# Optimization experiments

Measured on AMD Instinct MI355X. Metric: run time of the kernel, lower is better.

The kernel has to match this reference:

```python
import jax, jax.numpy as jnp
import numpy as np

RADIUS = 0.05
HMIN = -0.02
HMAX = 0.04
NSAMPLE = 64


def setup_inputs() -> dict:
    key = jax.random.key(0)
    k1, k2, k3, k4 = jax.random.split(key, 4)
    B, N, P, C = 2, 16384, 1024, 256
    xyz = jax.random.uniform(k1, (B, N, 3), dtype=jnp.float32)
    new_xyz = jax.random.uniform(k2, (B, P, 3), dtype=jnp.float32)
    rot = jax.random.normal(k3, (B, P, 3, 3), dtype=jnp.float32)
    features = jax.random.normal(k4, (B, C, N), dtype=jnp.float32)
    return {"xyz": xyz, "new_xyz": new_xyz, "rot": rot, "features": features}


def cylinder_query(xyz, new_xyz, rot):
    """Returns (B, P, NSAMPLE) int32 indices into the N axis of xyz.

    Faithful to the torch version: the torch code sorts all N candidates by
    distance (knn with K=N) and then top-k's a cylinder score over them; since
    the candidate set is all N points, this equals a direct top-k of the score
    over N (candidate ordering only affects float ties).
    """
    # delta = candidate point - center, in world frame: (B, P, N, 3)
    delta = xyz[:, None, :, :] - new_xyz[:, :, None, :]
    # rotate into cylinder frame: matmul(delta, rot^T) -> sum_d delta_d * rot[j, d]
    dcyl = jnp.einsum('bpnd,bpjd->bpnj', delta, rot)
    x, y, z = dcyl[..., 0], dcyl[..., 1], dcyl[..., 2]
    radial = jnp.sqrt(jnp.maximum(y * y + z * z, 0.0))
    in_cyl = (radial <= RADIUS) & (x >= HMIN) & (x <= HMAX)
    score = jnp.where(in_cyl, radial + 1e-3 * jnp.abs(x), jnp.inf)
    # smallest-score top-k via top_k on negated score
    neg_vals, pos = jax.lax.top_k(-score, NSAMPLE)  # (B, P, NSAMPLE)
    vals = -neg_vals
    # fallback: nearest point (torch uses idx_cand[..., 0], the KNN-nearest)
    d2 = jnp.sum(delta * delta, axis=-1)  # (B, P, N)
    fallback = jnp.argmin(d2, axis=-1)  # (B, P)
    no_valid = jnp.isinf(vals[..., 0])  # no point inside cylinder
    idx = jnp.where(no_valid[..., None], fallback[..., None], pos)
    return idx


def reference(xyz, new_xyz, rot, features):
    B = xyz.shape[0]
    idx = cylinder_query(xyz, new_xyz, rot)  # (B, P, S)
    # group xyz: (B, P, S, 3)
    grouped_xyz = jax.vmap(lambda p, i: p[i])(xyz, idx)
    grouped_xyz = grouped_xyz - new_xyz[:, :, None, :]
    # rotate_xyz: grouped @ rot  -> sum_d g_d * rot[d, e]
    grouped_xyz = jnp.einsum('bpsd,bpde->bpse', grouped_xyz, rot)
    grouped_xyz = jnp.transpose(grouped_xyz, (0, 3, 1, 2))  # (B, 3, P, S)
    # group features: (B, C, P, S)
    grouped_feat = jax.vmap(lambda f, i: f[:, i])(features, idx)
    return jnp.concatenate([grouped_xyz, grouped_feat], axis=1)  # (B, 3+C, P, S)
```

## Files before the change

kernel.cpp:

```cpp
#include <hip/hip_runtime.h>
#include <stdint.h>

#define B_ 2
#define N_ 16384
#define P_ 1024
#define C_ 256
#define S_ 64
#define CH_ (C_ + 3)
#define CAP_ 512

#define INF_BITS 0x7F800000u

typedef unsigned long long u64;

struct QS {
    u64 keys[CAP_];
    uint32_t hist[4][256];
    u64 red[4];
    uint32_t wsum[4];
    int vflag[128];
    int cnt;
    int sel;
    uint32_t k;
};

struct GT {
    uint32_t tileu[32][130];
};

union USmem {
    QS qs;
    GT g;
};

__device__ __forceinline__ u64 umin64(u64 a, u64 b) { return a < b ? a : b; }

__device__ __forceinline__ uint32_t f2bf(float f) {
    uint32_t x = __float_as_uint(f);
    return (x + 0x7fffu + ((x >> 16) & 1u)) >> 16;
}
__device__ __forceinline__ float bf2f(uint32_t u) { return __uint_as_float(u << 16); }

__device__ u64 block_min_u64(u64 v, u64* s_red) {
    int tid = threadIdx.x;
#pragma unroll
    for (int o = 32; o > 0; o >>= 1)
        v = umin64(v, (u64)__shfl_xor(v, o, 64));
    __syncthreads();
    if ((tid & 63) == 0) s_red[tid >> 6] = v;
    __syncthreads();
    u64 r = s_red[0];
#pragma unroll
    for (int w = 1; w < 4; ++w) r = umin64(r, s_red[w]);
    return r;
}

__device__ __forceinline__ uint32_t eval_sb(float px, float py, float pz,
                                            float cx, float cy, float cz,
                                            float r0, float r1, float r2,
                                            float r3, float r4, float r5,
                                            float r6, float r7, float r8) {
    float dx = px - cx, dy = py - cy, dz = pz - cz;
    float xr = __fadd_rn(__fadd_rn(__fmul_rn(dx, r0), __fmul_rn(dy, r1)), __fmul_rn(dz, r2));
    float yr = __fadd_rn(__fadd_rn(__fmul_rn(dx, r3), __fmul_rn(dy, r4)), __fmul_rn(dz, r5));
    float zr = __fadd_rn(__fadd_rn(__fmul_rn(dx, r6), __fmul_rn(dy, r7)), __fmul_rn(dz, r8));
    float rad2 = __fadd_rn(__fmul_rn(yr, yr), __fmul_rn(zr, zr));
    float radial = __fsqrt_rn(fmaxf(rad2, 0.0f));
    bool valid = (radial <= 0.05f) && (xr >= -0.02f) && (xr <= 0.04f);
    float score = __fadd_rn(radial, __fmul_rn(1e-3f, fabsf(xr)));
    return valid ? __float_as_uint(score) : INF_BITS;
}

__device__ __forceinline__ uint32_t score_bits(const float* __restrict__ xb, int n,
                                               float cx, float cy, float cz,
                                               float r0, float r1, float r2,
                                               float r3, float r4, float r5,
                                               float r6, float r7, float r8) {
    return eval_sb(xb[n * 3 + 0], xb[n * 3 + 1], xb[n * 3 + 2],
                   cx, cy, cz, r0, r1, r2, r3, r4, r5, r6, r7, r8);
}

__device__ void select_idx(QS& qs, const float* __restrict__ xb,
                           float cx, float cy, float cz,
                           float r0, float r1, float r2, float r3, float r4,
                           float r5, float r6, float r7, float r8,
                           int* s_out) {
    const int tid = threadIdx.x;
    const int wid = tid >> 6;
    const int v = qs.cnt;

    if (v == 0) {
        u64 fb = ~0ull;
        for (int n = tid; n < N_; n += 256) {
            float px = xb[n * 3 + 0], py = xb[n * 3 + 1], pz = xb[n * 3 + 2];
            float dx = px - cx, dy = py - cy, dz = pz - cz;
            float d2 = __fadd_rn(__fadd_rn(__fmul_rn(dx, dx), __fmul_rn(dy, dy)),
                                 __fmul_rn(dz, dz));
            fb = umin64(fb, ((u64)__float_as_uint(d2) << 32) | (unsigned)n);
        }
        u64 m = block_min_u64(fb, qs.red);
        if (tid < S_) s_out[tid] = (int)(unsigned)(m & 0xFFFFFFFFu);
    } else if (v <= 64) {
        if (tid >= v && tid < 64)
            qs.keys[tid] = 0xFFFFFFFF00000000ull | (unsigned)(0x10000 + tid);
        __syncthreads();
        u64 key = 0;
        int rank = 0;
        if (tid < 64) {
            key = qs.keys[tid];
            for (int o = 0; o < 64; ++o) rank += (qs.keys[o] < key) ? 1 : 0;
        }
        __syncthreads();
        if (tid < 64) qs.keys[rank] = key;
        __syncthreads();
        const int needed = 64 - v;
        if (tid < 64 && needed > 0) {
            bool inv0 = (qs.vflag[tid] == 0);
            u64 m0 = __ballot(inv0);
            int before0 = __popcll(m0 & ((1ull << tid) - 1ull));
            if (inv0 && before0 < needed) qs.keys[v + before0] = (unsigned)tid;
            int c0 = __popcll(m0);
            if (c0 < needed) {
                bool inv1 = (qs.vflag[64 + tid] == 0);
                u64 m1 = __ballot(inv1);
                int b1 = c0 + __popcll(m1 & ((1ull << tid) - 1ull));
                if (inv1 && b1 < needed) qs.keys[v + b1] = (unsigned)(64 + tid);
            }
        }
        __syncthreads();
        if (tid < S_) s_out[tid] = (int)(unsigned)(qs.keys[tid] & 0xFFFFFFFFu);
    } else if (v <= CAP_) {
        for (int i = tid; i < v; i += 256) {
            u64 key = qs.keys[i];
            int rank = 0;
            for (int j = 0; j < v; ++j) rank += (qs.keys[j] < key) ? 1 : 0;
            if (rank < 64) s_out[rank] = (int)(unsigned)(key & 0xFFFFFFFFu);
        }
    } else {
        uint32_t prefix = 0, mask = 0, kk = 64;
        for (int pass = 0; pass < 4; ++pass) {
            const int shift = 24 - 8 * pass;
            __syncthreads();
            qs.hist[0][tid] = 0;
            qs.hist[1][tid] = 0;
            qs.hist[2][tid] = 0;
            qs.hist[3][tid] = 0;
            __syncthreads();
            for (int n = tid; n < N_; n += 256) {
                uint32_t sb = score_bits(xb, n, cx, cy, cz, r0, r1, r2, r3, r4, r5, r6, r7, r8);
                if (sb != INF_BITS && (sb & mask) == prefix)
                    atomicAdd(&qs.hist[wid][(sb >> shift) & 255u], 1u);
            }
            __syncthreads();
            uint32_t cnt = qs.hist[0][tid] + qs.hist[1][tid] + qs.hist[2][tid] + qs.hist[3][tid];
            uint32_t x = cnt;
#pragma unroll
            for (int o = 1; o < 64; o <<= 1) {
                uint32_t y = __shfl_up(x, o, 64);
                if ((tid & 63) >= o) x += y;
            }
            if ((tid & 63) == 63) qs.wsum[wid] = x;
            __syncthreads();
            uint32_t woff = 0;
            for (int w = 0; w < wid; ++w) woff += qs.wsum[w];
            uint32_t incl = x + woff;
            uint32_t excl = incl - cnt;
            if (kk > excl && kk <= incl) {
                qs.sel = tid;
                qs.k = kk - excl;
            }
            __syncthreads();
            prefix |= ((uint32_t)qs.sel) << shift;
            mask |= 255u << shift;
            kk = qs.k;
        }
        const uint32_t T = prefix;

        __syncthreads();
        if (tid == 0) qs.cnt = 0;
        __syncthreads();
        for (int n = tid; n < N_; n += 256) {
            uint32_t sb = score_bits(xb, n, cx, cy, cz, r0, r1, r2, r3, r4, r5, r6, r7, r8);
            if (sb != INF_BITS && sb <= T) {
                int pos = atomicAdd(&qs.cnt, 1);
                if (pos < CAP_) qs.keys[pos] = ((u64)sb << 32) | (unsigned)n;
            }
        }
        __syncthreads();
        int c = qs.cnt;
        if (c > CAP_) c = CAP_;
        for (int i = tid; i < c; i += 256) {
            u64 key = qs.keys[i];
            int rank = 0;
            for (int j = 0; j < c; ++j) rank += (qs.keys[j] < key) ? 1 : 0;
            if (rank < 64) s_out[rank] = (int)(unsigned)(key & 0xFFFFFFFFu);
        }
    }
}

__global__ __launch_bounds__(256) void transpose_kernel(const float* __restrict__ feat,
                                                        ushort* __restrict__ featT) {
    int t = blockIdx.x;
    int b = t >> 10;
    int rem = t & 1023;
    int cblk = rem >> 8;
    int nblk = rem & 255;
    __shared__ float tile[64][65];
    int tid = threadIdx.x;
    for (int i = tid; i < 1024; i += 256) {
        int cy = i >> 4, nx4 = (i & 15) * 4;
        float4 v = *(const float4*)&feat[((size_t)(b * C_ + cblk * 64 + cy)) * N_ +
                                         nblk * 64 + nx4];
        tile[cy][nx4 + 0] = v.x;
        tile[cy][nx4 + 1] = v.y;
        tile[cy][nx4 + 2] = v.z;
        tile[cy][nx4 + 3] = v.w;
    }
    __syncthreads();
    for (int i = tid; i < 1024; i += 256) {
        int ny = i >> 4, c4 = i & 15;
        uint32_t lo = f2bf(tile[c4 * 4 + 0][ny]) | (f2bf(tile[c4 * 4 + 1][ny]) << 16);
        uint32_t hi = f2bf(tile[c4 * 4 + 2][ny]) | (f2bf(tile[c4 * 4 + 3][ny]) << 16);
        uint2 v;
        v.x = lo;
        v.y = hi;
        *(uint2*)&featT[((size_t)(b * N_ + nblk * 64 + ny)) * C_ + cblk * 64 + c4 * 4] = v;
    }
}

__global__ __launch_bounds__(256) void qg_kernel(const ushort* __restrict__ featT,
                                                 const float* __restrict__ features,
                                                 const float* __restrict__ xyz,
                                                 const float* __restrict__ new_xyz,
                                                 const float* __restrict__ rot,
                                                 float* __restrict__ out, int useT) {
    __shared__ USmem sm;
    __shared__ int s_idx[S_];
    const int tid = threadIdx.x;
    const int lane = tid & 63;
    const int bp = blockIdx.x;
    const int b = bp >> 10;
    const int p = bp & 1023;

    if (tid == 0) sm.qs.cnt = 0;

    const float cx = new_xyz[bp * 3 + 0];
    const float cy = new_xyz[bp * 3 + 1];
    const float cz = new_xyz[bp * 3 + 2];
    const float* R = rot + (size_t)bp * 9;
    const float r0 = R[0], r1 = R[1], r2 = R[2];
    const float r3 = R[3], r4 = R[4], r5 = R[5];
    const float r6 = R[6], r7 = R[7], r8 = R[8];

    __syncthreads();

    const float* xb = xyz + (size_t)b * N_ * 3;
    const float4* xb4 = (const float4*)xb;

    for (int it = 0; it < N_ / 1024; ++it) {
        int t4 = it * 256 + tid;
        float4 A = xb4[t4 * 3 + 0];
        float4 Bv = xb4[t4 * 3 + 1];
        float4 Cv = xb4[t4 * 3 + 2];
        int n0 = t4 * 4;

        uint32_t s0 = eval_sb(A.x, A.y, A.z, cx, cy, cz, r0, r1, r2, r3, r4, r5, r6, r7, r8);
        uint32_t s1 = eval_sb(A.w, Bv.x, Bv.y, cx, cy, cz, r0, r1, r2, r3, r4, r5, r6, r7, r8);
        uint32_t s2 = eval_sb(Bv.z, Bv.w, Cv.x, cx, cy, cz, r0, r1, r2, r3, r4, r5, r6, r7, r8);
        uint32_t s3 = eval_sb(Cv.y, Cv.z, Cv.w, cx, cy, cz, r0, r1, r2, r3, r4, r5, r6, r7, r8);

        if (it == 0 && tid < 32) {
            sm.qs.vflag[n0 + 0] = (s0 != INF_BITS) ? 1 : 0;
            sm.qs.vflag[n0 + 1] = (s1 != INF_BITS) ? 1 : 0;
            sm.qs.vflag[n0 + 2] = (s2 != INF_BITS) ? 1 : 0;
            sm.qs.vflag[n0 + 3] = (s3 != INF_BITS) ? 1 : 0;
        }
        uint32_t mn = min(min(s0, s1), min(s2, s3));
        if (__any(mn != INF_BITS)) {
            uint32_t sb[4] = {s0, s1, s2, s3};
#pragma unroll
            for (int j = 0; j < 4; ++j) {
                u64 m = __ballot(sb[j] != INF_BITS);
                if (m) {
                    int leader = __builtin_ctzll(m);
                    int cnt = __popcll(m);
                    int base = 0;
                    if (lane == leader) base = atomicAdd(&sm.qs.cnt, cnt);
                    base = __shfl(base, leader, 64);
                    if (sb[j] != INF_BITS) {
                        int pos = base + __popcll(m & ((1ull << lane) - 1ull));
                        if (pos < CAP_) sm.qs.keys[pos] = ((u64)sb[j] << 32) | (unsigned)(n0 + j);
                    }
                }
            }
        }
    }
    __syncthreads();

    select_idx(sm.qs, xb, cx, cy, cz, r0, r1, r2, r3, r4, r5, r6, r7, r8, s_idx);
    __syncthreads();

    if (tid < S_) {
        int n = s_idx[tid];
        const float* pt = xyz + ((size_t)b * N_ + n) * 3;
        float dx = pt[0] - cx;
        float dy = pt[1] - cy;
        float dz = pt[2] - cz;
        float g0 = __fadd_rn(__fadd_rn(__fmul_rn(dx, r0), __fmul_rn(dy, r3)), __fmul_rn(dz, r6));
        float g1 = __fadd_rn(__fadd_rn(__fmul_rn(dx, r1), __fmul_rn(dy, r4)), __fmul_rn(dz, r7));
        float g2 = __fadd_rn(__fadd_rn(__fmul_rn(dx, r2), __fmul_rn(dy, r5)), __fmul_rn(dz, r8));
        out[(((size_t)b * CH_ + 0) * P_ + p) * S_ + tid] = g0;
        out[(((size_t)b * CH_ + 1) * P_ + p) * S_ + tid] = g1;
        out[(((size_t)b * CH_ + 2) * P_ + p) * S_ + tid] = g2;
    }

    for (int h = 0; h < 2; ++h) {
        if (h) __syncthreads();
        if (useT) {
            for (int i = tid; i < 32 * 32; i += 256) {
                int sl = i >> 5, cq = i & 31;
                int n = s_idx[h * 32 + sl];
                uint4 v = *(const uint4*)&featT[((size_t)b * N_ + n) * C_ + cq * 8];
                *(uint4*)&sm.g.tileu[sl][cq * 4] = v;
            }
        } else {
            for (int i = tid; i < 32 * 128; i += 256) {
                int sl = i >> 7, cp = i & 127;
                int n = s_idx[h * 32 + sl];
                uint32_t u0 = f2bf(features[((size_t)b * C_ + 2 * cp + 0) * N_ + n]);
                uint32_t u1 = f2bf(features[((size_t)b * C_ + 2 * cp + 1) * N_ + n]);
                sm.g.tileu[sl][cp] = u0 | (u1 << 16);
            }
        }
        __syncthreads();
        for (int i = tid; i < (C_ / 2) * 8; i += 256) {
            int cp = i >> 3, q = i & 7;
            uint32_t u0 = sm.g.tileu[4 * q + 0][cp];
            uint32_t u1 = sm.g.tileu[4 * q + 1][cp];
            uint32_t u2 = sm.g.tileu[4 * q + 2][cp];
            uint32_t u3 = sm.g.tileu[4 * q + 3][cp];
            float4 lo, hi;
            lo.x = bf2f(u0 & 0xffffu); lo.y = bf2f(u1 & 0xffffu);
            lo.z = bf2f(u2 & 0xffffu); lo.w = bf2f(u3 & 0xffffu);
            hi.x = bf2f(u0 >> 16); hi.y = bf2f(u1 >> 16);
            hi.z = bf2f(u2 >> 16); hi.w = bf2f(u3 >> 16);
            size_t base0 = (((size_t)b * CH_ + 3 + 2 * cp) * P_ + p) * S_ + h * 32 + 4 * q;
            *(float4*)&out[base0] = lo;
            *(float4*)&out[base0 + (size_t)P_ * S_] = hi;
        }
    }
}

extern "C" void kernel_launch(void* const* d_in, const int* in_sizes, int n_in,
                              void* d_out, int out_size, void* d_ws, size_t ws_size,
                              hipStream_t stream) {
    const float* xyz = (const float*)d_in[0];
    const float* new_xyz = (const float*)d_in[1];
    const float* rot = (const float*)d_in[2];
    const float* features = (const float*)d_in[3];
    float* out = (float*)d_out;

    const size_t featT_bytes = (size_t)B_ * N_ * C_ * sizeof(ushort);
    const int useT = (ws_size >= featT_bytes) ? 1 : 0;

    ushort* featT = (ushort*)d_ws;

    if (useT) {
        transpose_kernel<<<2048, 256, 0, stream>>>(features, featT);
    }
    qg_kernel<<<B_ * P_, 256, 0, stream>>>(featT, features, xyz, new_xyz, rot, out, useT);
}
```

Measured before the change: 64.23 us.

## Add uniform grid binning to prune cylinder query candidates

Adds a bin_kernel that counting-sorts each batch's points into a 16^3 grid and records cell start offsets. The query kernel maps each cylinder's extent through the inverse rotation to a world-space box of cells and scores only the points in those cells, instead of scanning all N points per query. It falls back to the full scan when the matrix is near-singular or the box covers too many cells. It also sets launch bounds to 8 blocks per SM. The cost is an extra single-block-per-batch launch (only 2 blocks) running before the others, plus binary-search overhead and dependence on the workspace being large enough.

```diff
diff --git a/kernel.cpp b/kernel.cpp
--- a/kernel.cpp
+++ b/kernel.cpp
@@ -8,6 +8,8 @@
 #define S_ 64
 #define CH_ (C_ + 3)
 #define CAP_ 512
+#define G_ 16
+#define NC_ (G_ * G_ * G_)
 
 #define INF_BITS 0x7F800000u
 
@@ -195,6 +197,68 @@
             for (int j = 0; j < c; ++j) rank += (qs.keys[j] < key) ? 1 : 0;
             if (rank < 64) s_out[rank] = (int)(unsigned)(key & 0xFFFFFFFFu);
         }
+    }
+}
+
+__global__ __launch_bounds__(256) void bin_kernel(const float* __restrict__ xyz,
+                                                  float4* __restrict__ sortedPts,
+                                                  int* __restrict__ cellStart) {
+    __shared__ uint32_t hist[NC_];
+    __shared__ uint32_t wsum[4];
+    const int b = blockIdx.x;
+    const int tid = threadIdx.x;
+    const int lane = tid & 63, wid = tid >> 6;
+    const float* xb = xyz + (size_t)b * N_ * 3;
+
+    for (int i = tid; i < NC_; i += 256) hist[i] = 0;
+    __syncthreads();
+    for (int n = tid; n < N_; n += 256) {
+        float x = xb[n * 3 + 0], y = xb[n * 3 + 1], z = xb[n * 3 + 2];
+        int cx = min(max((int)(x * 16.0f), 0), 15);
+        int cy = min(max((int)(y * 16.0f), 0), 15);
+        int cz = min(max((int)(z * 16.0f), 0), 15);
+        atomicAdd(&hist[(cx * 16 + cy) * 16 + cz], 1u);
+    }
+    __syncthreads();
+    uint32_t vals[16];
+    uint32_t s = 0;
+#pragma unroll
+    for (int k = 0; k < 16; ++k) vals[k] = hist[tid * 16 + k];
+#pragma unroll
+    for (int k = 0; k < 16; ++k) {
+        uint32_t t = vals[k];
+        vals[k] = s;
+        s += t;
+    }
+    uint32_t x = s;
+#pragma unroll
+    for (int o = 1; o < 64; o <<= 1) {
+        uint32_t y = __shfl_up(x, o, 64);
+        if (lane >= o) x += y;
+    }
+    if (lane == 63) wsum[wid] = x;
+    __syncthreads();
+    uint32_t woff = 0;
+    for (int w = 0; w < wid; ++w) woff += wsum[w];
+    uint32_t chunk_excl = woff + x - s;
+    int* cs = cellStart + b * (NC_ + 1);
+#pragma unroll
+    for (int k = 0; k < 16; ++k) {
+        uint32_t v = vals[k] + chunk_excl;
+        hist[tid * 16 + k] = v;
+        cs[tid * 16 + k] = (int)v;
+    }
+    if (tid == 0) cs[NC_] = N_;
+    __syncthreads();
+    for (int n = tid; n < N_; n += 256) {
+        float px = xb[n * 3 + 0], py = xb[n * 3 + 1], pz = xb[n * 3 + 2];
+        int cx = min(max((int)(px * 16.0f), 0), 15);
+        int cy = min(max((int)(py * 16.0f), 0), 15);
+        int cz = min(max((int)(pz * 16.0f), 0), 15);
+        uint32_t pos = atomicAdd(&hist[(cx * 16 + cy) * 16 + cz], 1u);
+        float4 pt;
+        pt.x = px; pt.y = py; pt.z = pz; pt.w = __uint_as_float((unsigned)n);
+        sortedPts[(size_t)b * N_ + pos] = pt;
     }
 }
 
@@ -228,21 +292,26 @@
     }
 }
 
-__global__ __launch_bounds__(256) void qg_kernel(const ushort* __restrict__ featT,
-                                                 const float* __restrict__ features,
-                                                 const float* __restrict__ xyz,
-                                                 const float* __restrict__ new_xyz,
-                                                 const float* __restrict__ rot,
-                                                 float* __restrict__ out, int useT) {
+__global__ __launch_bounds__(256, 8) void qg_kernel(const ushort* __restrict__ featT,
+                                                    const float* __restrict__ features,
+                                                    const float* __restrict__ xyz,
+                                                    const float* __restrict__ new_xyz,
+                                                    const float* __restrict__ rot,
+                                                    const float4* __restrict__ sortedPts,
+                                                    const int* __restrict__ cellStart,
+                                                    float* __restrict__ out,
+                                                    int useT, int usePrune) {
     __shared__ USmem sm;
     __shared__ int s_idx[S_];
     const int tid = threadIdx.x;
     const int lane = tid & 63;
+    const int wid = tid >> 6;
     const int bp = blockIdx.x;
     const int b = bp >> 10;
     const int p = bp & 1023;
 
     if (tid == 0) sm.qs.cnt = 0;
+    for (int i = tid; i < 128; i += 256) sm.qs.vflag[i] = 0;
 
     const float cx = new_xyz[bp * 3 + 0];
     const float cy = new_xyz[bp * 3 + 1];
@@ -252,45 +321,138 @@
     const float r3 = R[3], r4 = R[4], r5 = R[5];
     const float r6 = R[6], r7 = R[7], r8 = R[8];
 
+    bool fullscan = (usePrune == 0);
+    int clo0 = 0, clo1 = 0, clo2 = 0, chi0 = 0, chi1 = 0, chi2 = 0;
+    if (!fullscan) {
+        float det = r0 * (r4 * r8 - r5 * r7) - r1 * (r3 * r8 - r5 * r6) +
+                    r2 * (r3 * r7 - r4 * r6);
+        if (!(fabsf(det) > 0.04f)) {
+            fullscan = true;
+        } else {
+            float id = 1.0f / det;
+            float i00 = (r4 * r8 - r5 * r7) * id, i01 = (r2 * r7 - r1 * r8) * id,
+                  i02 = (r1 * r5 - r2 * r4) * id;
+            float i10 = (r5 * r6 - r3 * r8) * id, i11 = (r0 * r8 - r2 * r6) * id,
+                  i12 = (r2 * r3 - r0 * r5) * id;
+            float i20 = (r3 * r7 - r4 * r6) * id, i21 = (r1 * r6 - r0 * r7) * id,
+                  i22 = (r0 * r4 - r1 * r3) * id;
+            float ct0 = cx + i00 * 0.01f, ct1 = cy + i10 * 0.01f, ct2 = cz + i20 * 0.01f;
+            float h0 = (fabsf(i00) * 0.03f + fabsf(i01) * 0.05f + fabsf(i02) * 0.05f) * 1.01f + 0.005f;
+            float h1 = (fabsf(i10) * 0.03f + fabsf(i11) * 0.05f + fabsf(i12) * 0.05f) * 1.01f + 0.005f;
+            float h2 = (fabsf(i20) * 0.03f + fabsf(i21) * 0.05f + fabsf(i22) * 0.05f) * 1.01f + 0.005f;
+            clo0 = min(max((int)floorf((ct0 - h0) * 16.0f), 0), 15);
+            chi0 = min(max((int)floorf((ct0 + h0) * 16.0f), 0), 15);
+            clo1 = min(max((int)floorf((ct1 - h1) * 16.0f), 0), 15);
+            chi1 = min(max((int)floorf((ct1 + h1) * 16.0f), 0), 15);
+            clo2 = min(max((int)floorf((ct2 - h2) * 16.0f), 0), 15);
+            chi2 = min(max((int)floorf((ct2 + h2) * 16.0f), 0), 15);
+            int ncells = (chi0 - clo0 + 1) * (chi1 - clo1 + 1) * (chi2 - clo2 + 1);
+            if (ncells > 512) fullscan = true;
+        }
+    }
+
     __syncthreads();
 
     const float* xb = xyz + (size_t)b * N_ * 3;
     const float4* xb4 = (const float4*)xb;
 
-    for (int it = 0; it < N_ / 1024; ++it) {
-        int t4 = it * 256 + tid;
-        float4 A = xb4[t4 * 3 + 0];
-        float4 Bv = xb4[t4 * 3 + 1];
-        float4 Cv = xb4[t4 * 3 + 2];
-        int n0 = t4 * 4;
-
-        uint32_t s0 = eval_sb(A.x, A.y, A.z, cx, cy, cz, r0, r1, r2, r3, r4, r5, r6, r7, r8);
-        uint32_t s1 = eval_sb(A.w, Bv.x, Bv.y, cx, cy, cz, r0, r1, r2, r3, r4, r5, r6, r7, r8);
-        uint32_t s2 = eval_sb(Bv.z, Bv.w, Cv.x, cx, cy, cz, r0, r1, r2, r3, r4, r5, r6, r7, r8);
-        uint32_t s3 = eval_sb(Cv.y, Cv.z, Cv.w, cx, cy, cz, r0, r1, r2, r3, r4, r5, r6, r7, r8);
-
-        if (it == 0 && tid < 32) {
-            sm.qs.vflag[n0 + 0] = (s0 != INF_BITS) ? 1 : 0;
-            sm.qs.vflag[n0 + 1] = (s1 != INF_BITS) ? 1 : 0;
-            sm.qs.vflag[n0 + 2] = (s2 != INF_BITS) ? 1 : 0;
-            sm.qs.vflag[n0 + 3] = (s3 != INF_BITS) ? 1 : 0;
-        }
-        uint32_t mn = min(min(s0, s1), min(s2, s3));
-        if (__any(mn != INF_BITS)) {
-            uint32_t sb[4] = {s0, s1, s2, s3};
-#pragma unroll
-            for (int j = 0; j < 4; ++j) {
-                u64 m = __ballot(sb[j] != INF_BITS);
-                if (m) {
-                    int leader = __builtin_ctzll(m);
-                    int cnt = __popcll(m);
-                    int base = 0;
-                    if (lane == leader) base = atomicAdd(&sm.qs.cnt, cnt);
-                    base = __shfl(base, leader, 64);
-                    if (sb[j] != INF_BITS) {
-                        int pos = base + __popcll(m & ((1ull << lane) - 1ull));
-                        if (pos < CAP_) sm.qs.keys[pos] = ((u64)sb[j] << 32) | (unsigned)(n0 + j);
+    if (fullscan) {
+        for (int it = 0; it < N_ / 1024; ++it) {
+            int t4 = it * 256 + tid;
+            float4 A = xb4[t4 * 3 + 0];
+            float4 Bv = xb4[t4 * 3 + 1];
+            float4 Cv = xb4[t4 * 3 + 2];
+            int n0 = t4 * 4;
+
+            uint32_t s0 = eval_sb(A.x, A.y, A.z, cx, cy, cz, r0, r1, r2, r3, r4, r5, r6, r7, r8);
+            uint32_t s1 = eval_sb(A.w, Bv.x, Bv.y, cx, cy, cz, r0, r1, r2, r3, r4, r5, r6, r7, r8);
+            uint32_t s2 = eval_sb(Bv.z, Bv.w, Cv.x, cx, cy, cz, r0, r1, r2, r3, r4, r5, r6, r7, r8);
+            uint32_t s3 = eval_sb(Cv.y, Cv.z, Cv.w, cx, cy, cz, r0, r1, r2, r3, r4, r5, r6, r7, r8);
+
+            if (it == 0 && tid < 32) {
+                sm.qs.vflag[n0 + 0] = (s0 != INF_BITS) ? 1 : 0;
+                sm.qs.vflag[n0 + 1] = (s1 != INF_BITS) ? 1 : 0;
+                sm.qs.vflag[n0 + 2] = (s2 != INF_BITS) ? 1 : 0;
+                sm.qs.vflag[n0 + 3] = (s3 != INF_BITS) ? 1 : 0;
+            }
+            uint32_t mn = min(min(s0, s1), min(s2, s3));
+            if (__any(mn != INF_BITS)) {
+                uint32_t sb[4] = {s0, s1, s2, s3};
+#pragma unroll
+                for (int j = 0; j < 4; ++j) {
+                    u64 m = __ballot(sb[j] != INF_BITS);
+                    if (m) {
+                        int leader = __builtin_ctzll(m);
+                        int cnt = __popcll(m);
+                        int base = 0;
+                        if (lane == leader) base = atomicAdd(&sm.qs.cnt, cnt);
+                        base = __shfl(base, leader, 64);
+                        if (sb[j] != INF_BITS) {
+                            int pos = base + __popcll(m & ((1ull << lane) - 1ull));
+                            if (pos < CAP_)
+                                sm.qs.keys[pos] = ((u64)sb[j] << 32) | (unsigned)(n0 + j);
+                        }
                     }
+                }
+            }
+        }
+    } else {
+        const int nyy = chi1 - clo1 + 1;
+        const int nruns = (chi0 - clo0 + 1) * nyy;
+        const int* cs = cellStart + b * (NC_ + 1);
+        if (tid < nruns) {
+            int ix = clo0 + tid / nyy;
+            int iy = clo1 + tid % nyy;
+            int cbase = (ix * 16 + iy) * 16;
+            int st = cs[cbase + clo2];
+            int en = cs[cbase + chi2 + 1];
+            sm.qs.hist[0][tid] = (uint32_t)st;
+            sm.qs.hist[1][tid] = (uint32_t)(en - st);
+        }
+        __syncthreads();
+        uint32_t len = (tid < nruns) ? sm.qs.hist[1][tid] : 0;
+        uint32_t xsc = len;
+#pragma unroll
+        for (int o = 1; o < 64; o <<= 1) {
+            uint32_t y = __shfl_up(xsc, o, 64);
+            if (lane >= o) xsc += y;
+        }
+        if (lane == 63) sm.qs.wsum[wid] = xsc;
+        __syncthreads();
+        uint32_t woff = 0;
+        for (int w = 0; w < wid; ++w) woff += sm.qs.wsum[w];
+        uint32_t incl = xsc + woff;
+        sm.qs.hist[2][tid] = incl - len;
+        if (tid == 255) sm.qs.k = incl;
+        __syncthreads();
+        const int M = (int)sm.qs.k;
+        const float4* sp = sortedPts + (size_t)b * N_;
+        for (int base = 0; base < M; base += 256) {
+            int t = base + tid;
+            uint32_t sb = INF_BITS;
+            unsigned n = 0;
+            if (t < M) {
+                int lo = 0, hi = nruns - 1;
+                while (lo < hi) {
+                    int mid = (lo + hi + 1) >> 1;
+                    if ((int)sm.qs.hist[2][mid] <= t) lo = mid; else hi = mid - 1;
+                }
+                int off = t - (int)sm.qs.hist[2][lo];
+                float4 pt = sp[sm.qs.hist[0][lo] + off];
+                n = __float_as_uint(pt.w);
+                sb = eval_sb(pt.x, pt.y, pt.z, cx, cy, cz, r0, r1, r2, r3, r4, r5, r6, r7, r8);
+                if (n < 128 && sb != INF_BITS) sm.qs.vflag[n] = 1;
+            }
+            u64 m = __ballot(sb != INF_BITS);
+            if (m) {
+                int leader = __builtin_ctzll(m);
+                int c2 = __popcll(m);
+                int basep = 0;
+                if (lane == leader) basep = atomicAdd(&sm.qs.cnt, c2);
+                basep = __shfl(basep, leader, 64);
+                if (sb != INF_BITS) {
+                    int pos = basep + __popcll(m & ((1ull << lane) - 1ull));
+                    if (pos < CAP_) sm.qs.keys[pos] = ((u64)sb << 32) | n;
                 }
             }
         }
@@ -361,12 +523,21 @@
     float* out = (float*)d_out;
 
     const size_t featT_bytes = (size_t)B_ * N_ * C_ * sizeof(ushort);
+    const size_t sorted_bytes = (size_t)B_ * N_ * sizeof(float4);
+    const size_t cells_bytes = (size_t)B_ * (NC_ + 1) * sizeof(int);
     const int useT = (ws_size >= featT_bytes) ? 1 : 0;
+    const int usePrune = (ws_size >= featT_bytes + sorted_bytes + cells_bytes) ? 1 : 0;
 
     ushort* featT = (ushort*)d_ws;
-
+    float4* sortedPts = (float4*)((char*)d_ws + featT_bytes);
+    int* cellStart = (int*)((char*)d_ws + featT_bytes + sorted_bytes);
+
+    if (usePrune) {
+        bin_kernel<<<B_, 256, 0, stream>>>(xyz, sortedPts, cellStart);
+    }
     if (useT) {
         transpose_kernel<<<2048, 256, 0, stream>>>(features, featT);
     }
-    qg_kernel<<<B_ * P_, 256, 0, stream>>>(featT, features, xyz, new_xyz, rot, out, useT);
-}
+    qg_kernel<<<B_ * P_, 256, 0, stream>>>(featT, features, xyz, new_xyz, rot,
+                                           sortedPts, cellStart, out, useT, usePrune);
+}
```

After: 86.71 us. 35.0% more time.
